# Optimization experiments

Hardware: AMD Instinct MI355X
Metric: run time of the kernel (lower is better)

Reference implementation:

```python
import jax, jax.numpy as jnp
import numpy as np
import math

B, S, D, H, C, A, SD, L, STEPS = 128, 256, 1024, 16, 50, 32, 64, 6, 10


def setup_inputs():
    key = jax.random.key(0)
    ks = jax.random.split(key, 16)
    rn = lambda k, sh, std=0.02: jax.random.normal(k, sh, jnp.float32) * std
    z = lambda sh: jnp.zeros(sh, jnp.float32)
    o = lambda sh: jnp.ones(sh, jnp.float32)
    return dict(
        reasoning=jax.random.normal(ks[0], (B, S, D), jnp.float32),
        state=jax.random.normal(ks[1], (B, SD), jnp.float32),
        x0=jax.random.normal(ks[2], (B, C, A), jnp.float32),
        W_se=rn(ks[3], (SD, D)), b_se=z(D), g_se=o(D), be_se=z(D),
        W_ap=rn(ks[4], (A, D)), b_ap=z(D),
        W_ad=rn(ks[5], (D, A), 0.001), b_ad=z(A),
        mem_latent=rn(ks[6], (1, 1, D)),
        Wq=rn(ks[7], (D, D)), bq=z(D), Wk=rn(ks[8], (D, D)), bk=z(D),
        Wv=rn(ks[9], (D, D)), bv=z(D), Wo=rn(ks[10], (D, D)), bo=z(D),
        g_q=o(D), be_q=z(D), g_kv=o(D), be_kv=z(D),
        W_fp=rn(ks[11], (D, D)), b_fp=z(D),
        pos_emb=rn(ks[12], (C, D)),
        filmW=rn(ks[13], (L, D, D)), filmb=z((L, D)), filmg=o((L, D)), filmbe=z((L, D)),
        filmWf=rn(ks[14], (L, D, 2 * D)), filmbf=z((L, 2 * D)),
        flow_steps=STEPS,
    )


def _ln(x, g, b):
    m = x.mean(-1, keepdims=True)
    v = jnp.mean((x - m) ** 2, -1, keepdims=True)
    return (x - m) * jax.lax.rsqrt(v + 1e-5) * g + b


def reference(reasoning, state, x0, W_se, b_se, g_se, be_se, W_ap, b_ap, W_ad, b_ad,
              mem_latent, Wq, bq, Wk, bk, Wv, bv, Wo, bo, g_q, be_q, g_kv, be_kv,
              W_fp, b_fp, pos_emb, filmW, filmb, filmg, filmbe, filmWf, filmbf, flow_steps):
    B_, C_, A_ = x0.shape
    D_ = W_ap.shape[1]
    dh = D_ // H
    # --- generate_mem: cross-attn from learned latent over [reasoning; state_enc] ---
    se = _ln(state @ W_se + b_se, g_se, be_se)[:, None, :]          # [B,1,D]
    kv = _ln(jnp.concatenate([reasoning, se], 1), g_kv, be_kv)      # [B,S+1,D]
    q = _ln(jnp.broadcast_to(mem_latent, (B_, 1, D_)), g_q, be_q)   # [B,1,D]
    qh = (q @ Wq + bq).reshape(B_, 1, H, dh)
    kh = (kv @ Wk + bk).reshape(B_, -1, H, dh)
    vh = (kv @ Wv + bv).reshape(B_, -1, H, dh)
    att = jax.nn.softmax(jnp.einsum('bqhd,bkhd->bhqk', qh, kh) / math.sqrt(dh), -1)
    mem = jnp.einsum('bhqk,bkhd->bqhd', att, vh).reshape(B_, 1, D_) @ Wo + bo
    film_vec = mem[:, 0] @ W_fp + b_fp                               # [B,D]
    cond = jnp.broadcast_to(film_vec[:, None, :], (B_, C_, D_)).reshape(B_ * C_, D_)
    half = D_ // 2
    freqs = jnp.exp(jnp.linspace(0.0, math.log(1000.0), half))

    def velocity(x_t, t):
        x = x_t @ W_ap + b_ap + pos_emb[None]                        # [B,C,D]
        targ = t[:, None] * freqs[None, :]
        temb = jnp.concatenate([jnp.sin(targ), jnp.cos(targ)], -1)   # [B,D]
        h = (x + temb[:, None, :]).reshape(B_ * C_, D_)

        def film_step(h, p):
            W, b, g, be, Wf, bf = p
            hh = _ln(h @ W + b, g, be)
            gamma, beta = jnp.split(cond @ Wf + bf, 2, -1)
            return jax.nn.gelu((1.0 + gamma) * hh + beta, approximate=False), None

        h, _ = jax.lax.scan(film_step, h, (filmW, filmb, filmg, filmbe, filmWf, filmbf))
        return (h @ W_ad + b_ad).reshape(B_, C_, A_)

    # --- flow-matching Euler integration (sample) ---
    dt = 1.0 / flow_steps
    ts = jnp.arange(flow_steps, dtype=jnp.float32) * dt

    def euler(x_t, tval):
        v = velocity(x_t, jnp.full((B_,), tval))
        return x_t + v * dt, None

    x_t, _ = jax.lax.scan(euler, x0, ts)
    return x_t
```

## Files before the change

### kernel.cpp

```cpp
#include <hip/hip_runtime.h>
#include <math.h>

#define NB 128
#define NS 256
#define ND 1024
#define NH 16
#define NC 50
#define NA 32
#define NSD 64
#define NL 6
#define NSTEPS 10
#define NM (NB*NC)
#define NKV (NS+1)

typedef unsigned short u16;
typedef short bf16x8 __attribute__((ext_vector_type(8)));
typedef float f32x4 __attribute__((ext_vector_type(4)));
typedef unsigned short us4 __attribute__((ext_vector_type(4)));
typedef unsigned short us8 __attribute__((ext_vector_type(8)));

typedef __attribute__((address_space(1))) const void* gas_p;
typedef __attribute__((address_space(3))) void* las_p;

__device__ __forceinline__ float b2f(u16 h) { return __uint_as_float(((unsigned int)h) << 16); }
__device__ __forceinline__ u16 f2b(float f) {
  unsigned int u = __float_as_uint(f);
  return (u16)((u + 0x7fffu + ((u >> 16) & 1u)) >> 16);
}
__device__ __forceinline__ void gld16(const void* g, void* l) {
  __builtin_amdgcn_global_load_lds((gas_p)g, (las_p)l, 16, 0, 0);
}

__device__ __forceinline__ float wredsum(float v) {
#pragma unroll
  for (int o = 32; o > 0; o >>= 1) v += __shfl_down(v, o, 64);
  return v;
}
__device__ __forceinline__ void bsum2(float& a, float& b, float* red, int t) {
  float ra = wredsum(a), rb = wredsum(b);
  if ((t & 63) == 0) { red[(t >> 6) * 2] = ra; red[(t >> 6) * 2 + 1] = rb; }
  __syncthreads();
  a = red[0] + red[2] + red[4] + red[6];
  b = red[1] + red[3] + red[5] + red[7];
  __syncthreads();
}

__global__ __launch_bounds__(512) void film_gemm(const u16* __restrict__ Ag,
                                                 const u16* __restrict__ Bg,
                                                 u16* __restrict__ Ug) {
  __shared__ __align__(16) char smemc[65536];
  u16* smemu = (u16*)smemc;
  const int t = threadIdx.x, lane = t & 63, w = t >> 6;
  const int rb_ = blockIdx.x;
  const int bid = (rb_ & 7) * 50 + (rb_ >> 3);
  const int tm = bid >> 3, tn = bid & 7;
  const u16* Ab = Ag + (size_t)tm * 128 * ND;
  const u16* Bb = Bg + (size_t)tn * 128 * ND;
  const int c0 = t, c1 = t + 512;
  const int sr0 = c0 >> 3, sq0 = (c0 & 7) ^ (sr0 & 7);
  const int sr1 = c1 >> 3, sq1 = (c1 & 7) ^ (sr1 & 7);
  const int wq = w & 3, ksel = w >> 2;
  const int wr = (wq >> 1) * 64, wc = (wq & 1) * 64;
  const int fr = lane & 15, f8 = lane >> 4, r7 = fr & 7;
  const int qp = ksel * 4 + f8;

  f32x4 acc[4][4];
#pragma unroll
  for (int m = 0; m < 4; ++m)
#pragma unroll
    for (int n = 0; n < 4; ++n)
#pragma unroll
      for (int j = 0; j < 4; ++j) acc[m][n][j] = 0.f;

#define STAGE_FG(bofs, k0)                                                      \
  gld16(Ab + (size_t)sr0 * ND + (k0) + sq0 * 8, smemu + (bofs) + w * 512);      \
  gld16(Ab + (size_t)sr1 * ND + (k0) + sq1 * 8, smemu + (bofs) + 4096 + w * 512); \
  gld16(Bb + (size_t)sr0 * ND + (k0) + sq0 * 8, smemu + 16384 + (bofs) + w * 512); \
  gld16(Bb + (size_t)sr1 * ND + (k0) + sq1 * 8, smemu + 16384 + (bofs) + 4096 + w * 512);

  STAGE_FG(0, 0)
  __syncthreads();

  for (int it = 0; it < 16; ++it) {
    const int bofs = (it & 1) * 8192;
    if (it < 15) { STAGE_FG(8192 - bofs, (it + 1) * 64) }
    const u16* Asc = smemu + bofs;
    const u16* Bsc = smemu + 16384 + bofs;
    bf16x8 af[4], bfv[4];
#pragma unroll
    for (int m = 0; m < 4; ++m) {
      const int row = wr + m * 16 + fr;
      af[m] = *(const bf16x8*)(Asc + row * 64 + (qp ^ r7) * 8);
    }
#pragma unroll
    for (int n = 0; n < 4; ++n) {
      const int row = wc + n * 16 + fr;
      bfv[n] = *(const bf16x8*)(Bsc + row * 64 + (qp ^ r7) * 8);
    }
#pragma unroll
    for (int m = 0; m < 4; ++m)
#pragma unroll
      for (int n = 0; n < 4; ++n)
        acc[m][n] = __builtin_amdgcn_mfma_f32_16x16x32_bf16(af[m], bfv[n], acc[m][n], 0, 0, 0);
    __syncthreads();
  }
#undef STAGE_FG

  float* Cred = (float*)smemc;
  if (w >= 4) {
    const int base = (w - 4) * 4096;
#pragma unroll
    for (int m = 0; m < 4; ++m)
#pragma unroll
      for (int n = 0; n < 4; ++n)
#pragma unroll
        for (int j = 0; j < 4; ++j)
          Cred[base + (m * 16 + f8 * 4 + j) * 64 + n * 16 + fr] = acc[m][n][j];
  }
  __syncthreads();
  if (w < 4) {
    const int base = w * 4096;
#pragma unroll
    for (int m = 0; m < 4; ++m)
#pragma unroll
      for (int n = 0; n < 4; ++n)
#pragma unroll
        for (int j = 0; j < 4; ++j)
          acc[m][n][j] += Cred[base + (m * 16 + f8 * 4 + j) * 64 + n * 16 + fr];
  }
  __syncthreads();
  u16* Cs = smemu;
  if (w < 4) {
#pragma unroll
    for (int m = 0; m < 4; ++m)
#pragma unroll
      for (int n = 0; n < 4; ++n)
#pragma unroll
        for (int j = 0; j < 4; ++j)
          Cs[(wr + m * 16 + f8 * 4 + j) * 128 + wc + n * 16 + fr] = f2b(acc[m][n][j]);
  }
  __syncthreads();
  {
    const int row = t >> 2, cb0 = (t & 3) * 32;
    u16* dst = Ug + (size_t)(tm * 128 + row) * ND + tn * 128 + cb0;
    const u16* srcl = Cs + row * 128 + cb0;
#pragma unroll
    for (int i = 0; i < 4; ++i) *(us8*)(dst + i * 8) = *(const us8*)(srcl + i * 8);
  }
}

__global__ __launch_bounds__(256) void bgemm(const u16* __restrict__ A, const int a_rstride,
    const int a_zoff, const u16* __restrict__ Bp, const long long b_zoff,
    const float* __restrict__ bias, const int bias_zoff, u16* __restrict__ C,
    const int c_rstride, const long long c_zoff) {
  __shared__ u16 As[4096];
  __shared__ u16 Bs[2048];
  const int t = threadIdx.x, wv = t >> 6, lane = t & 63;
  const int nt = blockIdx.x, z = blockIdx.y;
  const u16* Ab = A + (size_t)z * a_zoff;
  const u16* Bb = Bp + (size_t)z * b_zoff + (size_t)nt * 64 * ND;
  const int ca = wv * 128 + lane;
  const int ra0 = ca >> 2, qa0 = (ca & 3) * 8;
  const int ca1 = ca + 64;
  const int ra1 = ca1 >> 2, qa1 = (ca1 & 3) * 8;
  const int cbk = wv * 64 + lane;
  const int rb0 = cbk >> 2, qb0 = (cbk & 3) * 8;
  const int wr = (wv >> 1) * 64, wc = (wv & 1) * 32;
  const int fr = lane & 15, fq = (lane >> 4) * 8;

  f32x4 acc[4][2];
#pragma unroll
  for (int m = 0; m < 4; ++m)
#pragma unroll
    for (int n = 0; n < 2; ++n)
#pragma unroll
      for (int j = 0; j < 4; ++j) acc[m][n][j] = 0.f;

  for (int k0 = 0; k0 < ND; k0 += 32) {
    __syncthreads();
    gld16(Ab + (size_t)ra0 * a_rstride + k0 + qa0, As + wv * 1024);
    gld16(Ab + (size_t)ra1 * a_rstride + k0 + qa1, As + wv * 1024 + 512);
    gld16(Bb + (size_t)rb0 * ND + k0 + qb0, Bs + wv * 512);
    __syncthreads();
    bf16x8 af[4], bfv[2];
#pragma unroll
    for (int m = 0; m < 4; ++m) af[m] = *(const bf16x8*)(As + (wr + m * 16 + fr) * 32 + fq);
#pragma unroll
    for (int n = 0; n < 2; ++n) bfv[n] = *(const bf16x8*)(Bs + (wc + n * 16 + fr) * 32 + fq);
#pragma unroll
    for (int m = 0; m < 4; ++m)
#pragma unroll
      for (int n = 0; n < 2; ++n)
        acc[m][n] = __builtin_amdgcn_mfma_f32_16x16x32_bf16(af[m], bfv[n], acc[m][n], 0, 0, 0);
  }
  const int rb = wr + (lane >> 4) * 4;
#pragma unroll
  for (int n = 0; n < 2; ++n) {
    const int col = nt * 64 + wc + n * 16 + fr;
    const float bz = bias[(size_t)z * bias_zoff + col];
#pragma unroll
    for (int m = 0; m < 4; ++m)
#pragma unroll
      for (int j = 0; j < 4; ++j)
        C[(size_t)z * c_zoff + (size_t)(rb + m * 16 + j) * c_rstride + col] =
            f2b(acc[m][n][j] + bz);
  }
}

__global__ __launch_bounds__(256) void ln_film(const u16* __restrict__ U,
    const float* __restrict__ lb, const float* __restrict__ lg, const float* __restrict__ lbe,
    const u16* __restrict__ gbB, u16* __restrict__ Hout) {
  const int t = threadIdx.x, wv = t >> 6, lane = t & 63;
  const int row = blockIdx.x * 4 + wv;
  const int b = row / NC;
  const int d0 = lane * 16;
  const u16* up = U + (size_t)row * ND + d0;
  us8 u0 = *(const us8*)up;
  us8 u1 = *(const us8*)(up + 8);
  float lbv[16], lgv[16], lbev[16];
#pragma unroll
  for (int i = 0; i < 4; ++i) {
    *(f32x4*)&lbv[i * 4]  = *(const f32x4*)&lb[d0 + i * 4];
    *(f32x4*)&lgv[i * 4]  = *(const f32x4*)&lg[d0 + i * 4];
    *(f32x4*)&lbev[i * 4] = *(const f32x4*)&lbe[d0 + i * 4];
  }
  float x[16];
#pragma unroll
  for (int i = 0; i < 8; ++i) x[i] = b2f((u16)u0[i]) + lbv[i];
#pragma unroll
  for (int i = 0; i < 8; ++i) x[8 + i] = b2f((u16)u1[i]) + lbv[8 + i];
  float s = 0.f, q = 0.f;
#pragma unroll
  for (int i = 0; i < 16; ++i) { s += x[i]; q += x[i] * x[i]; }
#pragma unroll
  for (int o = 32; o > 0; o >>= 1) { s += __shfl_xor(s, o, 64); q += __shfl_xor(q, o, 64); }
  const float m = s * (1.f / ND);
  const float rstd = rsqrtf(q * (1.f / ND) - m * m + 1e-5f);
  const u16* gbb = gbB + (size_t)b * (2 * ND);
  us8 g0 = *(const us8*)(gbb + d0);
  us8 g1 = *(const us8*)(gbb + d0 + 8);
  us8 e0 = *(const us8*)(gbb + ND + d0);
  us8 e1 = *(const us8*)(gbb + ND + d0 + 8);
  us8 o0, o1;
#pragma unroll
  for (int i = 0; i < 16; ++i) {
    const float hh = (x[i] - m) * rstd * lgv[i] + lbev[i];
    const float ga = (i < 8) ? b2f((u16)g0[i]) : b2f((u16)g1[i - 8]);
    const float be = (i < 8) ? b2f((u16)e0[i]) : b2f((u16)e1[i - 8]);
    const float y = (1.f + ga) * hh + be;
    const float gl = 0.5f * y * (1.f + erff(y * 0.70710678118654752f));
    const u16 r = f2b(gl);
    if (i < 8) o0[i] = r; else o1[i - 8] = r;
  }
  u16* op = Hout + (size_t)row * ND + d0;
  *(us8*)op = o0;
  *(us8*)(op + 8) = o1;
}

__global__ __launch_bounds__(256) void h0_mfma(const float* __restrict__ X,
    const u16* __restrict__ WapP, const float* __restrict__ bt,
    const float* __restrict__ pos, u16* __restrict__ Hout) {
  __shared__ u16 As[4096];
  __shared__ u16 Bs[4096];
  __shared__ u16 Cs[16384];
  const int t = threadIdx.x, wv = t >> 6, lane = t & 63;
  const int r0 = blockIdx.x * 128, c0 = blockIdx.y * 128;
  {
    const int r = t >> 1, hh = (t & 1) * 16;
    const float* xp = X + (size_t)(r0 + r) * NA + hh;
    u16* ad = As + r * 32 + hh;
#pragma unroll
    for (int i = 0; i < 4; ++i) {
      const f32x4 v = *(const f32x4*)(xp + i * 4);
      us4 o;
#pragma unroll
      for (int j = 0; j < 4; ++j) o[j] = f2b(v[j]);
      *(us4*)(ad + i * 4) = o;
    }
  }
  const u16* Bb = WapP + (size_t)c0 * NA;
  {
    const int c = wv * 128 + lane;
    gld16(Bb + (size_t)(c >> 2) * NA + (c & 3) * 8, Bs + wv * 1024);
    const int c1 = c + 64;
    gld16(Bb + (size_t)(c1 >> 2) * NA + (c1 & 3) * 8, Bs + wv * 1024 + 512);
  }
  __syncthreads();
  const int wr = (wv >> 1) * 64, wc = (wv & 1) * 64;
  const int fr = lane & 15, fq = (lane >> 4) * 8;
  bf16x8 af[4], bfv[4];
#pragma unroll
  for (int m = 0; m < 4; ++m) af[m] = *(const bf16x8*)(As + (wr + m * 16 + fr) * 32 + fq);
#pragma unroll
  for (int n = 0; n < 4; ++n) bfv[n] = *(const bf16x8*)(Bs + (wc + n * 16 + fr) * 32 + fq);
  f32x4 acc[4][4];
#pragma unroll
  for (int m = 0; m < 4; ++m)
#pragma unroll
    for (int n = 0; n < 4; ++n) {
#pragma unroll
      for (int j = 0; j < 4; ++j) acc[m][n][j] = 0.f;
      acc[m][n] = __builtin_amdgcn_mfma_f32_16x16x32_bf16(af[m], bfv[n], acc[m][n], 0, 0, 0);
    }
#pragma unroll
  for (int n = 0; n < 4; ++n) {
    const int col = c0 + wc + n * 16 + fr;
    const float btv = bt[col];
#pragma unroll
    for (int m = 0; m < 4; ++m)
#pragma unroll
      for (int j = 0; j < 4; ++j) {
        const int lr = wr + m * 16 + (lane >> 4) * 4 + j;
        const int c = (r0 + lr) % NC;
        Cs[lr * 128 + wc + n * 16 + fr] = f2b(acc[m][n][j] + btv + pos[(size_t)c * ND + col]);
      }
  }
  __syncthreads();
  {
    const int row = t >> 1, cb0 = (t & 1) * 64;
    u16* dst = Hout + (size_t)(r0 + row) * ND + c0 + cb0;
    const u16* srcl = Cs + row * 128 + cb0;
#pragma unroll
    for (int i = 0; i < 8; ++i) *(us8*)(dst + i * 8) = *(const us8*)(srcl + i * 8);
  }
}

__global__ __launch_bounds__(256) void vx_kernel(const u16* __restrict__ Hf,
    const u16* __restrict__ WadP, const float* __restrict__ b_ad,
    const float* __restrict__ Xin, float* __restrict__ Xout) {
  const int t = threadIdx.x, wv = t >> 6, lane = t & 63;
  const int r0 = blockIdx.x * 64 + wv * 16;
  f32x4 a0, a1;
#pragma unroll
  for (int j = 0; j < 4; ++j) { a0[j] = 0.f; a1[j] = 0.f; }
  const u16* ap = Hf + (size_t)(r0 + (lane & 15)) * ND + (lane >> 4) * 8;
  const u16* bp = WadP + lane * 8;
#pragma unroll 4
  for (int kt = 0; kt < 32; ++kt) {
    bf16x8 av = *(const bf16x8*)(ap + kt * 32);
    bf16x8 w0 = *(const bf16x8*)(bp + (kt * 2 + 0) * 512);
    bf16x8 w1 = *(const bf16x8*)(bp + (kt * 2 + 1) * 512);
    a0 = __builtin_amdgcn_mfma_f32_16x16x32_bf16(av, w0, a0, 0, 0, 0);
    a1 = __builtin_amdgcn_mfma_f32_16x16x32_bf16(av, w1, a1, 0, 0, 0);
  }
  const int rr = r0 + (lane >> 4) * 4;
  const int c0 = lane & 15;
#pragma unroll
  for (int j = 0; j < 4; ++j) {
    const int row = rr + j;
    const int i0 = row * NA + c0;
    Xout[i0] = Xin[i0] + 0.1f * (a0[j] + b_ad[c0]);
    const int i1 = row * NA + 16 + c0;
    Xout[i1] = Xin[i1] + 0.1f * (a1[j] + b_ad[16 + c0]);
  }
}

__global__ __launch_bounds__(256) void packT(const float* __restrict__ src,
    const long long src_zoff, const int srcw, u16* __restrict__ dst,
    const long long dst_zoff) {
  __shared__ float tl[64 * 65];
  const int l = blockIdx.z, kt = blockIdx.y, nt = blockIdx.x;
  const int t = threadIdx.x;
  const float* s = src + (size_t)l * src_zoff + (size_t)(kt * 64) * srcw + nt * 64;
#pragma unroll
  for (int j = 0; j < 4; ++j) {
    const int f = (t + j * 256) * 4;
    const int r = f >> 6, c = f & 63;
    const f32x4 v = *(const f32x4*)&s[(size_t)r * srcw + c];
#pragma unroll
    for (int i = 0; i < 4; ++i) tl[r * 65 + c + i] = v[i];
  }
  __syncthreads();
  const int nn = t >> 2, kg = (t & 3) * 16;
  us8 o0, o1;
#pragma unroll
  for (int i = 0; i < 8; ++i) o0[i] = f2b(tl[(kg + i) * 65 + nn]);
#pragma unroll
  for (int i = 0; i < 8; ++i) o1[i] = f2b(tl[(kg + 8 + i) * 65 + nn]);
  u16* d = dst + (size_t)l * dst_zoff + (size_t)(nt * 64 + nn) * ND + kt * 64 + kg;
  *(us8*)d = o0;
  *(us8*)(d + 8) = o1;
}

__global__ __launch_bounds__(256) void prep_misc(const float* __restrict__ W_ap,
    const float* __restrict__ W_ad, u16* __restrict__ WapP, u16* __restrict__ WadP,
    const float* __restrict__ b_ap, float* __restrict__ bt) {
  const int id = blockIdx.x * 256 + threadIdx.x;
#pragma unroll
  for (int i = 0; i < 4; ++i) {
    const int e = id * 4 + i;
    const int n = e >> 5, k = e & 31;
    WapP[e] = f2b(W_ap[k * ND + n]);
  }
#pragma unroll
  for (int i = 0; i < 4; ++i) {
    const int e = id * 4 + i;
    const int kt = e >> 10, rem = e & 1023;
    const int at = rem >> 9, rem2 = rem & 511;
    const int ln = rem2 >> 3, j = rem2 & 7;
    const int k = kt * 32 + (ln >> 4) * 8 + j;
    const int col = at * 16 + (ln & 15);
    WadP[e] = f2b(W_ad[k * NA + col]);
  }
  if (id < 2560) {
#pragma unroll
    for (int i = 0; i < 4; ++i) {
      const int e = id * 4 + i;
      const int s = e >> 10, d = e & 1023;
      const double lam = 6.907755278982137 / 511.0;
      const double tt = 0.1 * (double)s;
      double v;
      if (d < 512) v = sin(tt * exp(lam * (double)d));
      else         v = cos(tt * exp(lam * (double)(d - 512)));
      bt[e] = (float)v + b_ap[d];
    }
  }
}

__global__ __launch_bounds__(256) void se_kernel(const float* __restrict__ state,
    const float* __restrict__ W_se, const float* __restrict__ b_se,
    const float* __restrict__ g_se, const float* __restrict__ be_se,
    float* __restrict__ se_d) {
  __shared__ float xs[NSD];
  __shared__ float red[8];
  const int b = blockIdx.x, t = threadIdx.x;
  if (t < NSD) xs[t] = state[b * NSD + t];
  __syncthreads();
  const int d0 = t * 4;
  float acc[4];
#pragma unroll
  for (int i = 0; i < 4; ++i) acc[i] = b_se[d0 + i];
  for (int k = 0; k < NSD; ++k) {
    const float xv = xs[k];
    const f32x4 wv = *(const f32x4*)&W_se[(size_t)k * ND + d0];
#pragma unroll
    for (int i = 0; i < 4; ++i) acc[i] += xv * wv[i];
  }
  float s = acc[0] + acc[1] + acc[2] + acc[3];
  float q = acc[0]*acc[0] + acc[1]*acc[1] + acc[2]*acc[2] + acc[3]*acc[3];
  bsum2(s, q, red, t);
  const float m = s * (1.f / ND);
  const float rstd = rsqrtf(q * (1.f / ND) - m * m + 1e-5f);
#pragma unroll
  for (int i = 0; i < 4; ++i)
    se_d[(size_t)b * ND + d0 + i] = (acc[i] - m) * rstd * g_se[d0 + i] + be_se[d0 + i];
}

__global__ __launch_bounds__(256) void q1_kernel(const float* __restrict__ lat,
    const float* __restrict__ g_q, const float* __restrict__ be_q, float* __restrict__ qn) {
  __shared__ float red[8];
  const int t = threadIdx.x;
  const int d0 = t * 4;
  const f32x4 x = *(const f32x4*)&lat[d0];
  float s = x[0] + x[1] + x[2] + x[3];
  float q = x[0]*x[0] + x[1]*x[1] + x[2]*x[2] + x[3]*x[3];
  bsum2(s, q, red, t);
  const float m = s * (1.f / ND);
  const float rstd = rsqrtf(q * (1.f / ND) - m * m + 1e-5f);
#pragma unroll
  for (int i = 0; i < 4; ++i)
    qn[d0 + i] = (x[i] - m) * rstd * g_q[d0 + i] + be_q[d0 + i];
}

__global__ __launch_bounds__(256) void q2_split(const float* __restrict__ qn,
    const float* __restrict__ Wq, float* __restrict__ part) {
  __shared__ float ql[64];
  const int cc = blockIdx.x, kc = blockIdx.y, t = threadIdx.x;
  if (t < 64) ql[t] = qn[kc * 64 + t];
  __syncthreads();
  const int c = cc * 256 + t;
  float acc = 0.f;
#pragma unroll 8
  for (int k = 0; k < 64; ++k) acc += ql[k] * Wq[(size_t)(kc * 64 + k) * ND + c];
  part[kc * ND + c] = acc;
}
__global__ __launch_bounds__(256) void q2_red(const float* __restrict__ part,
    const float* __restrict__ bq, float* __restrict__ qh) {
  const int c = blockIdx.x * 256 + threadIdx.x;
  float a = bq[c];
#pragma unroll
  for (int i = 0; i < 16; ++i) a += part[i * ND + c];
  qh[c] = a;
}

__global__ __launch_bounds__(256) void q3_kernel(const float* __restrict__ Wk,
    const float* __restrict__ bk, const float* __restrict__ qh,
    float* __restrict__ wTf, float* __restrict__ sb) {
  __shared__ float ql[ND];
  __shared__ float wl[4 * ND];
  const int t = threadIdx.x;
  *(f32x4*)&ql[t * 4] = *(const f32x4*)&qh[t * 4];
  const int d0 = blockIdx.x * 4;
  const float* src = Wk + (size_t)d0 * ND;
#pragma unroll
  for (int i = 0; i < 4; ++i)
    *(f32x4*)&wl[(i * 256 + t) * 4] = *(const f32x4*)&src[(size_t)(i * 256 + t) * 4];
  __syncthreads();
  if (t < 64) {
    const int dl = t >> 4, h = t & 15;
    const float* wr_ = wl + dl * ND + h * 64;
    const float* qr = ql + h * 64;
    float acc = 0.f;
#pragma unroll 8
    for (int j = 0; j < 64; ++j) acc += wr_[j] * qr[j];
    wTf[h * ND + d0 + dl] = acc * 0.125f;
  } else if (blockIdx.x == 0 && t >= 64 && t < 80) {
    const int h = t - 64;
    float sv = 0.f;
    for (int j = 0; j < 64; ++j) sv += bk[h * 64 + j] * ql[h * 64 + j];
    sb[h] = sv * 0.125f;
  }
}

__global__ __launch_bounds__(256) void q4_kernel(const float* __restrict__ wTf,
    const float* __restrict__ g_kv, const float* __restrict__ be_kv,
    const float* __restrict__ sb, u16* __restrict__ gwP, float* __restrict__ cgw,
    float* __restrict__ cbw) {
  __shared__ float red[8];
  const int h = blockIdx.x, t = threadIdx.x;
  float pg = 0.f, pb = 0.f;
  for (int d = t; d < ND; d += 256) {
    const float w = wTf[h * ND + d];
    const float gw = g_kv[d] * w;
    gwP[(d >> 5) * 512 + (h + 16 * ((d >> 3) & 3)) * 8 + (d & 7)] = f2b(gw);
    pg += gw;
    pb += be_kv[d] * w;
  }
  bsum2(pg, pb, red, t);
  if (t == 0) { cgw[h] = pg; cbw[h] = pb + sb[h]; }
}

__global__ __launch_bounds__(256) void scores3(const float* __restrict__ reasoning,
    const float* __restrict__ se_d, const u16* __restrict__ gwP,
    const float* __restrict__ cgw, const float* __restrict__ cbw,
    float* __restrict__ scores, float* __restrict__ stats) {
  __shared__ u16 gwl[16384];
  __shared__ float smv[4][16], srv[4][16];
  const int t = threadIdx.x, wv = t >> 6, lane = t & 63;
#pragma unroll
  for (int i = 0; i < 8; ++i)
    gld16(gwP + (i * 256 + t) * 8, gwl + i * 2048 + wv * 512);
  const int r0 = blockIdx.x * 64 + wv * 16;
  const int rowA = r0 + (lane & 15);
  const unsigned bA = (unsigned)rowA / NKV;
  const int kA = rowA - bA * NKV;
  const float* ptr = ((kA < NS) ? reasoning + ((size_t)bA * NS + kA) * ND
                                : se_d + (size_t)bA * ND) + (lane >> 4) * 8;
  __syncthreads();
  f32x4 acc;
#pragma unroll
  for (int j = 0; j < 4; ++j) acc[j] = 0.f;
  float s = 0.f, q = 0.f;
  for (int kt = 0; kt < 32; ++kt) {
    const f32x4 v0 = *(const f32x4*)(ptr + kt * 32);
    const f32x4 v1 = *(const f32x4*)(ptr + kt * 32 + 4);
    bf16x8 af;
#pragma unroll
    for (int j = 0; j < 4; ++j) {
      af[j] = (short)f2b(v0[j]);
      af[4 + j] = (short)f2b(v1[j]);
      s += v0[j] + v1[j];
      q += v0[j] * v0[j] + v1[j] * v1[j];
    }
    const bf16x8 bfr = *(const bf16x8*)(gwl + kt * 512 + lane * 8);
    acc = __builtin_amdgcn_mfma_f32_16x16x32_bf16(af, bfr, acc, 0, 0, 0);
  }
  s += __shfl_xor(s, 16, 64); s += __shfl_xor(s, 32, 64);
  q += __shfl_xor(q, 16, 64); q += __shfl_xor(q, 32, 64);
  const float m = s * (1.f / ND);
  const float rstd = rsqrtf(q * (1.f / ND) - m * m + 1e-5f);
  if (lane < 16) {
    smv[wv][lane] = m; srv[wv][lane] = rstd;
    const int row = r0 + lane;
    stats[(size_t)row * 2] = m;
    stats[(size_t)row * 2 + 1] = rstd;
  }
  __syncthreads();
  const int h = lane & 15;
  const float cg = cgw[h], cb = cbw[h];
#pragma unroll
  for (int j = 0; j < 4; ++j) {
    const int lr = (lane >> 4) * 4 + j;
    const int row = r0 + lr;
    const float mm = smv[wv][lr], rr = srv[wv][lr];
    const unsigned b = (unsigned)row / NKV;
    const int k = row - b * NKV;
    scores[((size_t)b * NH + h) * NKV + k] = rr * acc[j] - rr * mm * cg + cb;
  }
}

__global__ __launch_bounds__(256) void ctx2(const float* __restrict__ reasoning,
    const float* __restrict__ se_d, const float* __restrict__ scores,
    const float* __restrict__ stats, const float* __restrict__ g_kv,
    const float* __restrict__ be_kv, u16* __restrict__ ctxb) {
  __shared__ float sc[NH][260];
  __shared__ float stm[NKV], str[NKV];
  __shared__ float c1s[NH];
  const int chunk = blockIdx.x, b = blockIdx.y;
  const int t = threadIdx.x, wv = t >> 6, lane = t & 63;
#pragma unroll
  for (int h = 0; h < NH; ++h)
    for (int k = t; k < NKV; k += 256) sc[h][k] = scores[((size_t)b * NH + h) * NKV + k];
  for (int k = t; k < NKV; k += 256) {
    stm[k] = stats[((size_t)b * NKV + k) * 2];
    str[k] = stats[((size_t)b * NKV + k) * 2 + 1];
  }
  __syncthreads();
#pragma unroll
  for (int hh = 0; hh < 4; ++hh) {
    const int h = wv * 4 + hh;
    float mx = -1e30f;
    for (int i = 0; i < 5; ++i) { const int k = lane + i * 64; if (k < NKV) mx = fmaxf(mx, sc[h][k]); }
#pragma unroll
    for (int o = 32; o > 0; o >>= 1) mx = fmaxf(mx, __shfl_xor(mx, o, 64));
    float sm = 0.f;
    for (int i = 0; i < 5; ++i) {
      const int k = lane + i * 64;
      if (k < NKV) { const float e = __expf(sc[h][k] - mx); sc[h][k] = e; sm += e; }
    }
#pragma unroll
    for (int o = 32; o > 0; o >>= 1) sm += __shfl_xor(sm, o, 64);
    const float inv = 1.f / sm;
    float c1 = 0.f;
    for (int i = 0; i < 5; ++i) {
      const int k = lane + i * 64;
      if (k < NKV) {
        const float a = sc[h][k] * inv * str[k];
        sc[h][k] = a;
        c1 += a * stm[k];
      }
    }
#pragma unroll
    for (int o = 32; o > 0; o >>= 1) c1 += __shfl_xor(c1, o, 64);
    if (lane == 0) c1s[h] = c1;
  }
  __syncthreads();
  const int c = chunk * 256 + t;
  const float g = g_kv[c], be = be_kv[c];
  float acc[16];
#pragma unroll
  for (int h = 0; h < 16; ++h) acc[h] = 0.f;
  const float* xc = reasoning + (size_t)b * NS * ND + c;
#pragma unroll 2
  for (int k4 = 0; k4 < 64; ++k4) {
    const float x0 = xc[(size_t)(k4 * 4 + 0) * ND];
    const float x1 = xc[(size_t)(k4 * 4 + 1) * ND];
    const float x2 = xc[(size_t)(k4 * 4 + 2) * ND];
    const float x3 = xc[(size_t)(k4 * 4 + 3) * ND];
#pragma unroll
    for (int h = 0; h < 16; ++h) {
      const f32x4 w = *(const f32x4*)&sc[h][k4 * 4];
      acc[h] += w[0] * x0 + w[1] * x1 + w[2] * x2 + w[3] * x3;
    }
  }
  {
    const float xs = se_d[(size_t)b * ND + c];
#pragma unroll
    for (int h = 0; h < 16; ++h) acc[h] += sc[h][NS] * xs;
  }
#pragma unroll
  for (int h = 0; h < 16; ++h)
    ctxb[((size_t)b * NH + h) * ND + c] = f2b(g * (acc[h] - c1s[h]) + be);
}

extern "C" void kernel_launch(void* const* d_in, const int* in_sizes, int n_in,
                              void* d_out, int out_size, void* d_ws, size_t ws_size,
                              hipStream_t stream) {
  (void)in_sizes; (void)n_in; (void)out_size; (void)ws_size;
  const float* reasoning = (const float*)d_in[0];
  const float* state  = (const float*)d_in[1];
  const float* x0     = (const float*)d_in[2];
  const float* W_se   = (const float*)d_in[3];
  const float* b_se   = (const float*)d_in[4];
  const float* g_se   = (const float*)d_in[5];
  const float* be_se  = (const float*)d_in[6];
  const float* W_ap   = (const float*)d_in[7];
  const float* b_ap   = (const float*)d_in[8];
  const float* W_ad   = (const float*)d_in[9];
  const float* b_ad   = (const float*)d_in[10];
  const float* mem_latent = (const float*)d_in[11];
  const float* Wq = (const float*)d_in[12]; const float* bq = (const float*)d_in[13];
  const float* Wk = (const float*)d_in[14]; const float* bk = (const float*)d_in[15];
  const float* Wv = (const float*)d_in[16]; const float* bv = (const float*)d_in[17];
  const float* Wo = (const float*)d_in[18]; const float* bo = (const float*)d_in[19];
  const float* g_q  = (const float*)d_in[20]; const float* be_q  = (const float*)d_in[21];
  const float* g_kv = (const float*)d_in[22]; const float* be_kv = (const float*)d_in[23];
  const float* W_fp = (const float*)d_in[24]; const float* b_fp = (const float*)d_in[25];
  const float* pos_emb = (const float*)d_in[26];
  const float* filmW  = (const float*)d_in[27]; const float* filmb  = (const float*)d_in[28];
  const float* filmg  = (const float*)d_in[29]; const float* filmbe = (const float*)d_in[30];
  const float* filmWf = (const float*)d_in[31]; const float* filmbf = (const float*)d_in[32];

  char* base = (char*)d_ws;
  size_t off = 0;
  auto alloc = [&](size_t bytes) -> void* {
    void* p = base + off;
    off += (bytes + 255) & ~(size_t)255;
    return p;
  };
  u16*  Wpack   = (u16*)alloc((size_t)NL * ND * ND * 2);
  u16*  Wfp2    = (u16*)alloc((size_t)NL * 2 * ND * ND * 2);
  u16*  Wvp     = (u16*)alloc((size_t)ND * ND * 2);
  u16*  Wop     = (u16*)alloc((size_t)ND * ND * 2);
  u16*  Wfpp    = (u16*)alloc((size_t)ND * ND * 2);
  u16*  WapP    = (u16*)alloc((size_t)NA * ND * 2);
  u16*  WadP    = (u16*)alloc((size_t)32768 * 2);
  float* bt     = (float*)alloc((size_t)NSTEPS * ND * 4);
  float* se_d   = (float*)alloc((size_t)NB * ND * 4);
  float* qn     = (float*)alloc((size_t)ND * 4);
  float* qh     = (float*)alloc((size_t)ND * 4);
  float* part   = (float*)alloc((size_t)16 * ND * 4);
  float* wTf    = (float*)alloc((size_t)NH * ND * 4);
  float* sb     = (float*)alloc((size_t)NH * 4);
  u16*  gwP     = (u16*)alloc((size_t)NH * ND * 2);
  float* cgw    = (float*)alloc((size_t)NH * 4);
  float* cbw    = (float*)alloc((size_t)NH * 4);
  float* stats  = (float*)alloc((size_t)NB * NKV * 2 * 4);
  float* scores = (float*)alloc((size_t)NB * NH * NKV * 4);
  u16*  ctxb    = (u16*)alloc((size_t)NB * NH * ND * 2);
  u16*  mem_pre = (u16*)alloc((size_t)NB * ND * 2);
  u16*  memb    = (u16*)alloc((size_t)NB * ND * 2);
  u16*  fvb     = (u16*)alloc((size_t)NB * ND * 2);
  u16*  gbB     = (u16*)alloc((size_t)NL * NB * 2 * ND * 2);
  u16*  hbuf    = (u16*)alloc((size_t)NM * ND * 2);
  u16*  ubuf    = (u16*)alloc((size_t)NM * ND * 2);

  packT<<<dim3(16, 16, NL), 256, 0, stream>>>(filmW, (long long)ND * ND, ND, Wpack,
                                              (long long)ND * ND);
  packT<<<dim3(32, 16, NL), 256, 0, stream>>>(filmWf, (long long)ND * 2 * ND, 2 * ND, Wfp2,
                                              (long long)2 * ND * ND);
  packT<<<dim3(16, 16, 1), 256, 0, stream>>>(Wv, 0, ND, Wvp, 0);
  packT<<<dim3(16, 16, 1), 256, 0, stream>>>(Wo, 0, ND, Wop, 0);
  packT<<<dim3(16, 16, 1), 256, 0, stream>>>(W_fp, 0, ND, Wfpp, 0);
  prep_misc<<<32, 256, 0, stream>>>(W_ap, W_ad, WapP, WadP, b_ap, bt);

  se_kernel<<<NB, 256, 0, stream>>>(state, W_se, b_se, g_se, be_se, se_d);
  q1_kernel<<<1, 256, 0, stream>>>(mem_latent, g_q, be_q, qn);
  q2_split<<<dim3(4, 16), 256, 0, stream>>>(qn, Wq, part);
  q2_red<<<4, 256, 0, stream>>>(part, bq, qh);
  q3_kernel<<<256, 256, 0, stream>>>(Wk, bk, qh, wTf, sb);
  q4_kernel<<<NH, 256, 0, stream>>>(wTf, g_kv, be_kv, sb, gwP, cgw, cbw);
  scores3<<<(NB * NKV) / 64, 256, 0, stream>>>(reasoning, se_d, gwP, cgw, cbw, scores, stats);
  ctx2<<<dim3(4, NB), 256, 0, stream>>>(reasoning, se_d, scores, stats, g_kv, be_kv, ctxb);
  bgemm<<<dim3(1, 16), 256, 0, stream>>>(ctxb, NH * ND, ND, Wvp, (long long)64 * ND, bv, 64,
                                         mem_pre, ND, 64);
  bgemm<<<dim3(16, 1), 256, 0, stream>>>(mem_pre, ND, 0, Wop, 0, bo, 0, memb, ND, 0);
  bgemm<<<dim3(16, 1), 256, 0, stream>>>(memb, ND, 0, Wfpp, 0, b_fp, 0, fvb, ND, 0);
  bgemm<<<dim3(32, NL), 256, 0, stream>>>(fvb, ND, 0, Wfp2, (long long)2 * ND * ND, filmbf,
                                          2 * ND, gbB, 2 * ND, (long long)NB * 2 * ND);

  for (int s = 0; s < NSTEPS; ++s) {
    const float* xin = (s == 0) ? x0 : (const float*)d_out;
    h0_mfma<<<dim3(NM / 128, 8), 256, 0, stream>>>(xin, WapP, bt + (size_t)s * ND, pos_emb,
                                                   hbuf);
    for (int l = 0; l < NL; ++l) {
      film_gemm<<<400, 512, 0, stream>>>(hbuf, Wpack + (size_t)l * ND * ND, ubuf);
      ln_film<<<NM / 4, 256, 0, stream>>>(ubuf, filmb + (size_t)l * ND, filmg + (size_t)l * ND,
                                          filmbe + (size_t)l * ND,
                                          gbB + (size_t)l * NB * 2 * ND, hbuf);
    }
    vx_kernel<<<NM / 64, 256, 0, stream>>>(hbuf, WadP, b_ad, xin, (float*)d_out);
  }
}
```

Before: 2.552 ms.

## Triple-buffer A tiles in film GEMM with vmcnt-gated barriers

Restructures the FiLM GEMM main loop. A tiles are now prefetched two k-steps ahead into a three-slot LDS ring, while B stays double-buffered. The full __syncthreads is replaced by an explicit s_waitcnt vmcnt(2) plus s_barrier, so the most recent A prefetch can stay in flight across the barrier. This should hide more global-load latency behind MFMA work, at the cost of 80KB of LDS instead of 64KB and a hand-written loop prologue and epilogue that depend on exact load ordering.

```diff
diff --git a/kernel.cpp b/kernel.cpp
--- a/kernel.cpp
+++ b/kernel.cpp
@@ -48,7 +48,7 @@
 __global__ __launch_bounds__(512) void film_gemm(const u16* __restrict__ Ag,
                                                  const u16* __restrict__ Bg,
                                                  u16* __restrict__ Ug) {
-  __shared__ __align__(16) char smemc[65536];
+  __shared__ __align__(16) char smemc[81920];
   u16* smemu = (u16*)smemc;
   const int t = threadIdx.x, lane = t & 63, w = t >> 6;
   const int rb_ = blockIdx.x;
@@ -72,39 +72,56 @@
 #pragma unroll
       for (int j = 0; j < 4; ++j) acc[m][n][j] = 0.f;
 
-#define STAGE_FG(bofs, k0)                                                      \
-  gld16(Ab + (size_t)sr0 * ND + (k0) + sq0 * 8, smemu + (bofs) + w * 512);      \
-  gld16(Ab + (size_t)sr1 * ND + (k0) + sq1 * 8, smemu + (bofs) + 4096 + w * 512); \
-  gld16(Bb + (size_t)sr0 * ND + (k0) + sq0 * 8, smemu + 16384 + (bofs) + w * 512); \
-  gld16(Bb + (size_t)sr1 * ND + (k0) + sq1 * 8, smemu + 16384 + (bofs) + 4096 + w * 512);
-
-  STAGE_FG(0, 0)
-  __syncthreads();
-
-  for (int it = 0; it < 16; ++it) {
-    const int bofs = (it & 1) * 8192;
-    if (it < 15) { STAGE_FG(8192 - bofs, (it + 1) * 64) }
-    const u16* Asc = smemu + bofs;
-    const u16* Bsc = smemu + 16384 + bofs;
-    bf16x8 af[4], bfv[4];
-#pragma unroll
-    for (int m = 0; m < 4; ++m) {
-      const int row = wr + m * 16 + fr;
-      af[m] = *(const bf16x8*)(Asc + row * 64 + (qp ^ r7) * 8);
-    }
-#pragma unroll
-    for (int n = 0; n < 4; ++n) {
-      const int row = wc + n * 16 + fr;
-      bfv[n] = *(const bf16x8*)(Bsc + row * 64 + (qp ^ r7) * 8);
-    }
-#pragma unroll
-    for (int m = 0; m < 4; ++m)
-#pragma unroll
-      for (int n = 0; n < 4; ++n)
-        acc[m][n] = __builtin_amdgcn_mfma_f32_16x16x32_bf16(af[m], bfv[n], acc[m][n], 0, 0, 0);
-    __syncthreads();
-  }
-#undef STAGE_FG
+#define STAGE_A(bi, k0)                                                           \
+  gld16(Ab + (size_t)sr0 * ND + (k0) + sq0 * 8, smemu + (bi) * 8192 + w * 512);   \
+  gld16(Ab + (size_t)sr1 * ND + (k0) + sq1 * 8, smemu + (bi) * 8192 + 4096 + w * 512);
+#define STAGE_B(bj, k0)                                                           \
+  gld16(Bb + (size_t)sr0 * ND + (k0) + sq0 * 8, smemu + 24576 + (bj) * 8192 + w * 512); \
+  gld16(Bb + (size_t)sr1 * ND + (k0) + sq1 * 8, smemu + 24576 + (bj) * 8192 + 4096 + w * 512);
+#define COMPUTE_IT(it)                                                            \
+  {                                                                               \
+    const u16* Asc = smemu + ((it) % 3) * 8192;                                   \
+    const u16* Bsc = smemu + 24576 + ((it) & 1) * 8192;                           \
+    bf16x8 af[4], bfv[4];                                                         \
+    _Pragma("unroll")                                                             \
+    for (int m = 0; m < 4; ++m)                                                   \
+      af[m] = *(const bf16x8*)(Asc + (wr + m * 16 + fr) * 64 + (qp ^ r7) * 8);    \
+    _Pragma("unroll")                                                             \
+    for (int n = 0; n < 4; ++n)                                                   \
+      bfv[n] = *(const bf16x8*)(Bsc + (wc + n * 16 + fr) * 64 + (qp ^ r7) * 8);   \
+    _Pragma("unroll")                                                             \
+    for (int m = 0; m < 4; ++m)                                                   \
+      _Pragma("unroll")                                                           \
+      for (int n = 0; n < 4; ++n)                                                 \
+        acc[m][n] = __builtin_amdgcn_mfma_f32_16x16x32_bf16(af[m], bfv[n],        \
+                                                            acc[m][n], 0, 0, 0); \
+  }
+#define PIPE_BARRIER(N)                                                           \
+  asm volatile("s_waitcnt vmcnt(" #N ")" ::: "memory");                           \
+  __builtin_amdgcn_sched_barrier(0);                                              \
+  __builtin_amdgcn_s_barrier();                                                   \
+  __builtin_amdgcn_sched_barrier(0);
+
+  STAGE_B(0, 0)
+  STAGE_A(0, 0)
+  STAGE_A(1, 64)
+  PIPE_BARRIER(2)
+
+  for (int it = 0; it < 14; ++it) {
+    STAGE_B((it + 1) & 1, (it + 1) * 64)
+    STAGE_A((it + 2) % 3, (it + 2) * 64)
+    COMPUTE_IT(it)
+    PIPE_BARRIER(2)
+  }
+  STAGE_B(1, 960)
+  COMPUTE_IT(14)
+  PIPE_BARRIER(0)
+  COMPUTE_IT(15)
+  __syncthreads();
+#undef STAGE_A
+#undef STAGE_B
+#undef COMPUTE_IT
+#undef PIPE_BARRIER
 
   float* Cred = (float*)smemc;
   if (w >= 4) {
```

Result: faster. 2.495 ms (median of 2 runs) (-2.2%).
